# Kernel tuning notes

Measured on AMD Instinct MI355X. Metric: run time of the kernel, lower is better.

The kernel has to match this reference:

```python
import jax, jax.numpy as jnp
import numpy as np
import math

SCOPE = 27
RICKER_WIDTH = 4.0
DAMP = 0.12
IN_CHANNELS = 128
BATCH, H, W = 64, 64, 64


def _mexican_hat(scope, std, damping):
    # Ricker (mexican hat) wavelet sampled on integer grid centered at scope//2,
    # matching weight_initialization.mexican_hat(scope, std, damping).
    x = np.arange(scope, dtype=np.float32) - scope // 2
    a = 2.0 / (np.sqrt(3.0 * std) * np.pi ** 0.25)
    wavelet = a * (1.0 - (x / std) ** 2) * np.exp(-(x ** 2) / (2.0 * std ** 2))
    return (damping * wavelet).astype(np.float32)


def setup_inputs() -> dict:
    key = jax.random.key(0)
    activations = jax.random.normal(key, (BATCH, IN_CHANNELS, H, W), dtype=jnp.float32)
    inhibition_filter = jnp.asarray(_mexican_hat(SCOPE, RICKER_WIDTH, DAMP)).reshape(1, 1, SCOPE)
    return {"activations": activations, "inhibition_filter": inhibition_filter}


def reference(activations, inhibition_filter):
    # activations: (N, C, H, W); inhibition_filter: (1, 1, scope)
    C = activations.shape[1]
    scope = inhibition_filter.shape[-1]

    # pad_roll: zero-pad filter to length C, roll so center lands at index 0 side
    pad_left = (C - scope) // 2
    pad_right = C - scope - pad_left
    k = jnp.concatenate([
        jnp.zeros((pad_left,), dtype=inhibition_filter.dtype),
        inhibition_filter[0, 0],
        jnp.zeros((pad_right,), dtype=inhibition_filter.dtype),
    ])
    k = jnp.roll(k, C // 2 + 1)  # (C,)

    # kronecker delta along channels
    delta = jnp.zeros((C,), dtype=activations.dtype).at[0].set(1.0)

    # frequency-domain deconvolution along the channel axis
    Fk = jnp.fft.fft(delta - k)  # (C,) complex
    sig = jnp.transpose(activations, (0, 2, 3, 1))  # NCHW -> NHWC
    out = jnp.fft.ifft(jnp.fft.fft(sig, axis=-1) / Fk, axis=-1).real
    return jnp.transpose(out, (0, 3, 1, 2)).astype(activations.dtype)
```

## Files before the change

### kernel.cpp

```cpp
#include <hip/hip_runtime.h>


typedef short bf16x8 __attribute__((ext_vector_type(8)));
typedef float f32x4 __attribute__((ext_vector_type(4)));

#define MFMA16x16x32 __builtin_amdgcn_mfma_f32_16x16x32_bf16

__device__ __forceinline__ unsigned short f2bf(float f) {
  union { float f; unsigned u; } v; v.f = f;
  unsigned u = v.u;
  u += 0x7fffu + ((u >> 16) & 1u);
  return (unsigned short)(u >> 16);
}

__global__ void build_g(const float* __restrict__ filt, float* __restrict__ g) {
  __shared__ float ct[128], st[128], fr[128], fi[128];
  const int t = threadIdx.x;
  const float ang = (float)t * 0.049087385212340526f;
  float s, c;
  __sincosf(ang, &s, &c);
  ct[t] = c; st[t] = s;
  __syncthreads();

  float re = 1.f, im = 0.f;
  for (int tt = 0; tt < 27; ++tt) {
    const int j = (115 + tt) & 127;
    const int idx = (j * t) & 127;
    const float kv = filt[tt];
    re -= kv * ct[idx];
    im += kv * st[idx];
  }
  fr[t] = re; fi[t] = im;
  __syncthreads();

  float acc = 0.f;
  for (int m = 0; m < 128; ++m) {
    const int idx = (m * t) & 127;
    const float dr = fr[m], di = fi[m];
    acc += (ct[idx] * dr + st[idx] * di) / (dr * dr + di * di);
  }
  g[t] = acc * (1.0f / 128.0f);
}

__global__ __launch_bounds__(256) void conv_inhib(
    const float* __restrict__ X, const float* __restrict__ gtab,
    float* __restrict__ Y) {
  __shared__ __align__(16) unsigned short Xt[128 * 136];
  __shared__ float gs[128];

  const int tid = threadIdx.x;
  const int l = tid & 63;
  const int w = tid >> 6;
  const int lane15 = l & 15;
  const int quad = l >> 4;

  const int bid = blockIdx.x;
  const int nimg = bid >> 5;
  const int s0 = (bid & 31) << 7;
  const float* Xn = X + (size_t)nimg * (128 * 4096);
  float* Yn = Y + (size_t)nimg * (128 * 4096);

  if (tid < 128) gs[tid] = gtab[tid];

  {
    const int ssub = (tid & 31) << 2;
    const int cbase = tid >> 5;
#pragma unroll
    for (int r = 0; r < 16; ++r) {
      const int c = cbase + (r << 3);
      const float4 v = *(const float4*)(Xn + (size_t)c * 4096 + s0 + ssub);
      unsigned short* dst = &Xt[c];
      dst[(ssub + 0) * 136] = f2bf(v.x);
      dst[(ssub + 1) * 136] = f2bf(v.y);
      dst[(ssub + 2) * 136] = f2bf(v.z);
      dst[(ssub + 3) * 136] = f2bf(v.w);
    }
  }
  __syncthreads();

  bf16x8 afrag[2][4];
#pragma unroll
  for (int i = 0; i < 2; ++i) {
    const int m = (w << 5) + (i << 4) + lane15;
#pragma unroll
    for (int kk = 0; kk < 4; ++kk) {
      const int kbase = (kk << 5) + (quad << 3);
#pragma unroll
      for (int j = 0; j < 8; ++j) {
        afrag[i][kk][j] = (short)f2bf(gs[(m - (kbase + j)) & 127]);
      }
    }
  }

  f32x4 acc[2][8];
#pragma unroll
  for (int i = 0; i < 2; ++i)
#pragma unroll
    for (int ns = 0; ns < 8; ++ns)
      acc[i][ns] = (f32x4){0.f, 0.f, 0.f, 0.f};

#pragma unroll
  for (int ns = 0; ns < 8; ++ns) {
    const int srow = (ns << 4) + lane15;
#pragma unroll
    for (int kk = 0; kk < 4; ++kk) {
      const bf16x8 b = *(const bf16x8*)&Xt[srow * 136 + (kk << 5) + (quad << 3)];
      acc[0][ns] = MFMA16x16x32(afrag[0][kk], b, acc[0][ns], 0, 0, 0);
      acc[1][ns] = MFMA16x16x32(afrag[1][kk], b, acc[1][ns], 0, 0, 0);
    }
  }

#pragma unroll
  for (int i = 0; i < 2; ++i) {
#pragma unroll
    for (int r = 0; r < 4; ++r) {
      const int c = (w << 5) + (i << 4) + (quad << 2) + r;
      float* Yc = Yn + (size_t)c * 4096 + s0 + lane15;
#pragma unroll
      for (int ns = 0; ns < 8; ++ns) {
        Yc[ns << 4] = acc[i][ns][r];
      }
    }
  }
}

extern "C" void kernel_launch(void* const* d_in, const int* in_sizes, int n_in,
                              void* d_out, int out_size, void* d_ws, size_t ws_size,
                              hipStream_t stream) {
  const float* act = (const float*)d_in[0];
  const float* filt = (const float*)d_in[1];
  float* out = (float*)d_out;
  float* g = (float*)d_ws;

  build_g<<<1, 128, 0, stream>>>(filt, g);
  conv_inhib<<<2048, 256, 0, stream>>>(act, g, out);
}
```

Measured before the change: 246.3 us.

## Drop LDS transpose; load activations directly into MFMA fragments per wave

Each wave now handles a 16-position spatial tile. It loads activation columns straight from global memory into bf16 MFMA A-fragments and uses the circulant structure to reuse 8 precomputed filter fragments rotated across output tiles. This removes the shared-memory staging, the bank-conflicting transposed writes and the block-wide barrier, and raises occupancy through launch bounds and a doubled grid. In exchange, global loads become 64-byte strided segments per channel and there is less latency hiding within each wave.

Measured after the change: 251.2 us. About the same (+2.0%).

```diff
diff --git a/kernel.cpp b/kernel.cpp
--- a/kernel.cpp
+++ b/kernel.cpp
@@ -42,85 +42,58 @@
   g[t] = acc * (1.0f / 128.0f);
 }
 
-__global__ __launch_bounds__(256) void conv_inhib(
+__global__ __launch_bounds__(256, 4) void conv_inhib(
     const float* __restrict__ X, const float* __restrict__ gtab,
     float* __restrict__ Y) {
-  __shared__ __align__(16) unsigned short Xt[128 * 136];
-  __shared__ float gs[128];
-
   const int tid = threadIdx.x;
   const int l = tid & 63;
   const int w = tid >> 6;
   const int lane15 = l & 15;
   const int quad = l >> 4;
 
-  const int bid = blockIdx.x;
-  const int nimg = bid >> 5;
-  const int s0 = (bid & 31) << 7;
-  const float* Xn = X + (size_t)nimg * (128 * 4096);
-  float* Yn = Y + (size_t)nimg * (128 * 4096);
+  const int mtile = (blockIdx.x << 2) + w;
+  const int sg = mtile << 4;
+  const int img = sg >> 12;
+  const int spos = sg & 4095;
 
-  if (tid < 128) gs[tid] = gtab[tid];
+  const float* Xn = X + (size_t)img * (128 * 4096) + spos + lane15;
+  float* Yn = Y + (size_t)img * (128 * 4096) + spos + (quad << 2);
 
-  {
-    const int ssub = (tid & 31) << 2;
-    const int cbase = tid >> 5;
+  bf16x8 gf[8];
 #pragma unroll
-    for (int r = 0; r < 16; ++r) {
-      const int c = cbase + (r << 3);
-      const float4 v = *(const float4*)(Xn + (size_t)c * 4096 + s0 + ssub);
-      unsigned short* dst = &Xt[c];
-      dst[(ssub + 0) * 136] = f2bf(v.x);
-      dst[(ssub + 1) * 136] = f2bf(v.y);
-      dst[(ssub + 2) * 136] = f2bf(v.z);
-      dst[(ssub + 3) * 136] = f2bf(v.w);
-    }
-  }
-  __syncthreads();
-
-  bf16x8 afrag[2][4];
+  for (int d = 0; d < 8; ++d) {
+    const int base = (d << 4) + lane15 - (quad << 3);
 #pragma unroll
-  for (int i = 0; i < 2; ++i) {
-    const int m = (w << 5) + (i << 4) + lane15;
-#pragma unroll
-    for (int kk = 0; kk < 4; ++kk) {
-      const int kbase = (kk << 5) + (quad << 3);
-#pragma unroll
-      for (int j = 0; j < 8; ++j) {
-        afrag[i][kk][j] = (short)f2bf(gs[(m - (kbase + j)) & 127]);
-      }
+    for (int j = 0; j < 8; ++j) {
+      gf[d][j] = (short)f2bf(gtab[(base - j) & 127]);
     }
   }
 
-  f32x4 acc[2][8];
+  f32x4 acc[8];
 #pragma unroll
-  for (int i = 0; i < 2; ++i)
-#pragma unroll
-    for (int ns = 0; ns < 8; ++ns)
-      acc[i][ns] = (f32x4){0.f, 0.f, 0.f, 0.f};
+  for (int nt = 0; nt < 8; ++nt) acc[nt] = (f32x4){0.f, 0.f, 0.f, 0.f};
 
 #pragma unroll
-  for (int ns = 0; ns < 8; ++ns) {
-    const int srow = (ns << 4) + lane15;
+  for (int kt = 0; kt < 4; ++kt) {
+    const float* Xk = Xn + (size_t)((kt << 5) + (quad << 3)) * 4096;
+    float xa[8];
 #pragma unroll
-    for (int kk = 0; kk < 4; ++kk) {
-      const bf16x8 b = *(const bf16x8*)&Xt[srow * 136 + (kk << 5) + (quad << 3)];
-      acc[0][ns] = MFMA16x16x32(afrag[0][kk], b, acc[0][ns], 0, 0, 0);
-      acc[1][ns] = MFMA16x16x32(afrag[1][kk], b, acc[1][ns], 0, 0, 0);
+    for (int j = 0; j < 8; ++j) xa[j] = Xk[(size_t)j * 4096];
+    bf16x8 af;
+#pragma unroll
+    for (int j = 0; j < 8; ++j) af[j] = (short)f2bf(xa[j]);
+#pragma unroll
+    for (int nt = 0; nt < 8; ++nt) {
+      acc[nt] = MFMA16x16x32(af, gf[(nt - (kt << 1)) & 7], acc[nt], 0, 0, 0);
     }
   }
 
 #pragma unroll
-  for (int i = 0; i < 2; ++i) {
-#pragma unroll
-    for (int r = 0; r < 4; ++r) {
-      const int c = (w << 5) + (i << 4) + (quad << 2) + r;
-      float* Yc = Yn + (size_t)c * 4096 + s0 + lane15;
-#pragma unroll
-      for (int ns = 0; ns < 8; ++ns) {
-        Yc[ns << 4] = acc[i][ns][r];
-      }
-    }
+  for (int nt = 0; nt < 8; ++nt) {
+    const int c = (nt << 4) + lane15;
+    float4 v;
+    v.x = acc[nt][0]; v.y = acc[nt][1]; v.z = acc[nt][2]; v.w = acc[nt][3];
+    *(float4*)(Yn + (size_t)c * 4096) = v;
   }
 }
 
@@ -133,5 +106,5 @@
   float* g = (float*)d_ws;
 
   build_g<<<1, 128, 0, stream>>>(filt, g);
-  conv_inhib<<<2048, 256, 0, stream>>>(act, g, out);
+  conv_inhib<<<4096, 256, 0, stream>>>(act, g, out);
 }
```
